# Kernel tuning notes

Measured on AMD Instinct MI355X. Metric: run time of the kernel, lower is better.

## Reference

```python
import jax, jax.numpy as jnp
from jax import lax
import numpy as np

FRAME_LEN = 128
HOP = 64  # frame_len // 2 (default hop)
SAMPLE_LEN = 65536
IR_LEN = 1024

# torch.hann_window(N) is periodic: 0.5*(1 - cos(2*pi*n/N))
WIN = 0.5 * (1.0 - jnp.cos(2.0 * jnp.pi * jnp.arange(FRAME_LEN, dtype=jnp.float32) / FRAME_LEN))


def setup_inputs() -> dict:
    key = jax.random.key(0)
    k1, k2 = jax.random.split(key)
    x = jax.random.normal(k1, (1, SAMPLE_LEN), dtype=jnp.float32)
    IR = jax.random.normal(k2, (1, IR_LEN), dtype=jnp.float32)
    return {"x": x, "IR": IR}


def _scale_ir(ir2d):
    # get_MSG + scale_IR(target_gain = MSG + 2)
    spec = jnp.fft.rfft(ir2d[0])
    mag = jnp.abs(spec)
    phase = jnp.angle(spec)
    power = mag ** 2
    MLG = jnp.mean(power)
    zero_phase = (phase > -0.1) & (phase < 0.1)  # DC bin always qualifies
    peak_gain = jnp.max(jnp.where(zero_phase, power, -jnp.inf))
    MSG = -10.0 * jnp.log10(peak_gain / MLG)
    target_gain = MSG + 2.0
    mean_gain = 10.0 * jnp.log10(MLG)
    factor = jnp.power(jnp.float32(0.5), (target_gain - mean_gain) / 6.0)
    return ir2d / factor


def _howling(x1d, ir1d):
    L = x1d.shape[0]
    conv_len = FRAME_LEN + ir1d.shape[0] - 1
    # number of iterations that perform the feedback update (torch loop breaks
    # when frame_start + conv_len >= sample_len, AFTER adding to howling_out)
    n_fb = max(0, (L - conv_len - 1) // HOP)

    def step(x, i):
        fs = i * HOP
        frame = lax.dynamic_slice(x, (fs,), (FRAME_LEN,))
        w = WIN * frame
        conv = jnp.convolve(w, ir1d)  # mode='full', length conv_len
        fs2 = fs + HOP
        seg = lax.dynamic_slice(x, (fs2,), (conv_len,)) + conv
        x = lax.dynamic_update_slice(x, seg, (fs2,))
        x = jnp.clip(x, -1.0, 1.0)
        return x, w

    x_out, frames = lax.scan(step, x1d, jnp.arange(n_fb))
    # last iteration: windowed frame added to howling_out, then break (no feedback, no clamp)
    fs_last = n_fb * HOP
    last_w = WIN * lax.dynamic_slice(x_out, (fs_last,), (FRAME_LEN,))
    frames = jnp.concatenate([frames, last_w[None, :]], axis=0)  # [T, frame_len]
    T = n_fb + 1
    pos = (jnp.arange(T)[:, None] * HOP + jnp.arange(FRAME_LEN)[None, :]).reshape(-1)
    howl = jnp.zeros((L,), x1d.dtype).at[pos].add(frames.reshape(-1))
    return jnp.clip(howl, -1.0, 1.0)


def reference(x, IR):
    ir = _scale_ir(IR)
    out = _howling(x[0], ir[0])
    return out[None, :]
```

## Files before the change

### kernel.cpp

```cpp
#include <hip/hip_runtime.h>
#include <math.h>

#define FRAME 128
#define HOPW 64
#define SLEN 65536
#define IRLEN 1024
#define NFB 1006
#define RMASK 2047
#define PI_D 3.14159265358979323846

__device__ __forceinline__ float clip1(float v) { return fminf(1.0f, fmaxf(-1.0f, v)); }

__device__ __forceinline__ void loop_barrier() {
    __builtin_amdgcn_sched_barrier(0);
    asm volatile("s_waitcnt lgkmcnt(0)" ::: "memory");
    __builtin_amdgcn_s_barrier();
    __builtin_amdgcn_sched_barrier(0);
}

__global__ __launch_bounds__(768) void howl_fused(const float* __restrict__ x,
                                                  const float* __restrict__ ir,
                                                  float* __restrict__ out) {
    __shared__ float ring[2048];
    __shared__ float part[3][4][1152];
    __shared__ float irl[IRLEN];
    __shared__ float tailb[2][HOPW];
    __shared__ float red1[1024];
    __shared__ float red2[1024];
    __shared__ float invfs;

    const int tid = threadIdx.x;
    const int lane = tid & 63;
    const int wvid = tid >> 6;
    const int kg = tid / 192;
    const int ob = tid % 192;
    const int q = ob * 6;
    const int lo = q - kg * 32 - 31;
    const int s = kg * 32 + (lane & 31);

    for (int idx = tid; idx < IRLEN; idx += 768) irl[idx] = ir[idx];
    for (int idx = tid; idx < 1216; idx += 768) ring[idx] = x[idx];
    if (tid >= 513) { red1[tid] = -INFINITY; red2[tid] = 0.f; }
    if (tid < 256) { red1[768 + tid] = -INFINITY; red2[768 + tid] = 0.f; }
    __syncthreads();

    if (tid < 513) {
        double th = -2.0 * PI_D * (double)tid / 1024.0;
        double c4 = cos(4.0 * th), s4 = sin(4.0 * th);
        double wr0 = 1.0,           wi0 = 0.0;
        double wr1 = cos(th),       wi1 = sin(th);
        double wr2 = cos(2.0 * th), wi2 = sin(2.0 * th);
        double wr3 = cos(3.0 * th), wi3 = sin(3.0 * th);
        double ar0 = 0, ai0 = 0, ar1 = 0, ai1 = 0, ar2 = 0, ai2 = 0, ar3 = 0, ai3 = 0;
        for (int m = 0; m < 256; ++m) {
            double x0 = irl[4 * m], x1 = irl[4 * m + 1], x2 = irl[4 * m + 2], x3 = irl[4 * m + 3];
            ar0 += x0 * wr0; ai0 += x0 * wi0;
            ar1 += x1 * wr1; ai1 += x1 * wi1;
            ar2 += x2 * wr2; ai2 += x2 * wi2;
            ar3 += x3 * wr3; ai3 += x3 * wi3;
            double t;
            t = wr0 * c4 - wi0 * s4; wi0 = wr0 * s4 + wi0 * c4; wr0 = t;
            t = wr1 * c4 - wi1 * s4; wi1 = wr1 * s4 + wi1 * c4; wr1 = t;
            t = wr2 * c4 - wi2 * s4; wi2 = wr2 * s4 + wi2 * c4; wr2 = t;
            t = wr3 * c4 - wi3 * s4; wi3 = wr3 * s4 + wi3 * c4; wr3 = t;
        }
        double re = (ar0 + ar1) + (ar2 + ar3);
        double im = (ai0 + ai1) + (ai2 + ai3);
        float mag = (float)sqrt(re * re + im * im);
        float pw = mag * mag;
        double ph = atan2(im, re);
        int ok = (ph > -0.1 && ph < 0.1) ? 1 : 0;
        red1[tid] = ok ? pw : -INFINITY;
        red2[tid] = pw;
    }
    __syncthreads();
    for (int st = 512; st > 0; st >>= 1) {
        if (tid < st) {
            red1[tid] = fmaxf(red1[tid], red1[tid + st]);
            red2[tid] = red2[tid] + red2[tid + st];
        }
        __syncthreads();
    }
    if (tid == 0) {
        float peak = red1[0];
        float MLG = red2[0] / 513.0f;
        float MSG = -10.0f * log10f(peak / MLG);
        float target_gain = MSG + 2.0f;
        float mean_gain = 10.0f * log10f(MLG);
        invfs = powf(0.5f, (target_gain - mean_gain) / 6.0f);
    }
    __syncthreads();

    const float fbc = invfs;
    float wir[37];
#pragma unroll
    for (int j = 0; j < 37; ++j) {
        int idx = lo + j;
        wir[j] = (idx >= 0 && idx < IRLEN) ? irl[idx] / fbc : 0.f;
    }

    const float hwv = (float)(0.5 * (1.0 - cos(PI_D * (double)s / 64.0)));

    float wreg = hwv * ring[s];
    if ((wvid == 0 || wvid == 3) && lane < 32) out[s] = clip1(wreg);
    if ((wvid == 6 || wvid == 9) && lane < 32) tailb[0][s - 64] = wreg;
    float xv = 0.f;
    if (wvid == 4) xv = x[1216 + lane];
    __syncthreads();

    auto body = [&](int i, float (*cur)[1152], const float (*prev)[1152], int first) {
        const int base = i * HOPW;

        if (wvid == 4) {
            int pos = base + 1216 + lane;
            if (pos < SLEN) ring[pos & RMASK] = clip1(xv);
            int np = pos + HOPW;
            xv = (np < SLEN) ? x[np] : 0.f;
        }

        if (!first && (wvid == 2 || wvid == 5 || wvid == 8 || wvid == 11)) {
            int c = ((wvid - 2) / 3) * 64 + lane;
            int p = 128 + 4 * c;
            float4 g0 = *(const float4*)&prev[0][p];
            float4 g1 = *(const float4*)&prev[1][p];
            float4 g2 = *(const float4*)&prev[2][p];
            float4 g3 = *(const float4*)&prev[3][p];
            int slot = (base + p) & RMASK;
            float4 r = *(float4*)&ring[slot];
            r.x = clip1(r.x + (((g0.x + g1.x) + g2.x) + g3.x));
            r.y = clip1(r.y + (((g0.y + g1.y) + g2.y) + g3.y));
            r.z = clip1(r.z + (((g0.z + g1.z) + g2.z) + g3.z));
            r.w = clip1(r.w + (((g0.w + g1.w) + g2.w) + g3.w));
            *(float4*)&ring[slot] = r;
        }

        float a0 = 0, a1 = 0, a2 = 0, a3 = 0, a4 = 0, a5 = 0;
#pragma unroll
        for (int kk = 0; kk < 32; ++kk) {
            float sc = __int_as_float(__builtin_amdgcn_readlane(__float_as_int(wreg), 31 - kk));
            a0 = fmaf(sc, wir[kk + 0], a0);
            a1 = fmaf(sc, wir[kk + 1], a1);
            a2 = fmaf(sc, wir[kk + 2], a2);
            a3 = fmaf(sc, wir[kk + 3], a3);
            a4 = fmaf(sc, wir[kk + 4], a4);
            a5 = fmaf(sc, wir[kk + 5], a5);
        }
        float* pw = &cur[kg][q];
        *(float2*)(pw + 0) = make_float2(a0, a1);
        *(float2*)(pw + 2) = make_float2(a2, a3);
        *(float2*)(pw + 4) = make_float2(a4, a5);

        loop_barrier();

        float rr = ring[(base + 64 + s) & RMASK];
        float c0 = cur[0][s], c1 = cur[1][s], c2 = cur[2][s], c3 = cur[3][s];
        float sc4 = ((c0 + c1) + c2) + c3;
        if (kg < 2) {
            float v;
            if (first) {
                v = clip1(rr + sc4);
            } else {
                float m0 = prev[0][64 + s], m1 = prev[1][64 + s];
                float m2 = prev[2][64 + s], m3 = prev[3][64 + s];
                float sm = ((m0 + m1) + m2) + m3;
                v = clip1(clip1(rr + sm) + sc4);
            }
            float wn = hwv * v;
            if ((wvid == 0 || wvid == 3) && lane < 32) {
                float told = tailb[i & 1][s];
                out[base + 64 + s] = clip1(wn + told);
            }
            wreg = wn;
        } else {
            float v = clip1(rr + sc4);
            float wn = hwv * v;
            if ((wvid == 6 || wvid == 9) && lane < 32) tailb[(i + 1) & 1][s - 64] = wn;
            wreg = wn;
        }
    };

    float (*P0)[1152] = part[0];
    float (*P1)[1152] = part[1];
    float (*P2)[1152] = part[2];

    body(0, P0, P2, 1);
#pragma unroll 1
    for (int i = 1; i < NFB; i += 3) {
        body(i,     P1, P0, 0);
        body(i + 1, P2, P1, 0);
        body(i + 2, P0, P2, 0);
    }

    if ((wvid == 6 || wvid == 9) && lane < 32) out[64448 + (s - 64)] = clip1(wreg);
    for (int idx = 64512 + tid; idx < SLEN; idx += 768) out[idx] = 0.f;
}

extern "C" void kernel_launch(void* const* d_in, const int* in_sizes, int n_in,
                              void* d_out, int out_size, void* d_ws, size_t ws_size,
                              hipStream_t stream) {
    const float* x = (const float*)d_in[0];
    const float* ir = (const float*)d_in[1];
    float* out = (float*)d_out;
    (void)d_ws; (void)ws_size; (void)in_sizes; (void)n_in; (void)out_size;

    hipLaunchKernelGGL(howl_fused, dim3(1), dim3(768), 0, stream, x, ir, out);
}
```

Before: 1.144 ms.

## Replace triple-buffered single-barrier pipeline with two-barrier loop through LDS

The rotating three-buffer partial-sum scheme, which needed one barrier per step, is replaced by a single partial buffer. Each step now ends with a second barrier, after the ring update and the next windowed frame are written to LDS. The next frame is passed through a shared wlds array instead of staying in registers, the output accumulation moves to wave 0, and waves 0-1 get raised scheduling priority. The code is simpler, but each iteration now has two block-wide barriers on the serial critical path instead of one.

```diff
diff --git a/kernel.cpp b/kernel.cpp
--- a/kernel.cpp
+++ b/kernel.cpp
@@ -21,10 +21,10 @@
 __global__ __launch_bounds__(768) void howl_fused(const float* __restrict__ x,
                                                   const float* __restrict__ ir,
                                                   float* __restrict__ out) {
-    __shared__ float ring[2048];
-    __shared__ float part[3][4][1152];
+    __shared__ __align__(16) float ring[2048];
+    __shared__ __align__(16) float part[4][1152];
     __shared__ float irl[IRLEN];
-    __shared__ float tailb[2][HOPW];
+    __shared__ float wlds[FRAME];
     __shared__ float red1[1024];
     __shared__ float red2[1024];
     __shared__ float invfs;
@@ -36,7 +36,6 @@
     const int ob = tid % 192;
     const int q = ob * 6;
     const int lo = q - kg * 32 - 31;
-    const int s = kg * 32 + (lane & 31);
 
     for (int idx = tid; idx < IRLEN; idx += 768) irl[idx] = ir[idx];
     for (int idx = tid; idx < 1216; idx += 768) ring[idx] = x[idx];
@@ -90,8 +89,8 @@
         invfs = powf(0.5f, (target_gain - mean_gain) / 6.0f);
     }
     __syncthreads();
+    const float fbc = invfs;
 
-    const float fbc = invfs;
     float wir[37];
 #pragma unroll
     for (int j = 0; j < 37; ++j) {
@@ -99,41 +98,31 @@
         wir[j] = (idx >= 0 && idx < IRLEN) ? irl[idx] / fbc : 0.f;
     }
 
-    const float hwv = (float)(0.5 * (1.0 - cos(PI_D * (double)s / 64.0)));
+    const float hvs = (float)(0.5 * (1.0 - cos(PI_D * (double)(tid & 127) / 64.0)));
 
-    float wreg = hwv * ring[s];
-    if ((wvid == 0 || wvid == 3) && lane < 32) out[s] = clip1(wreg);
-    if ((wvid == 6 || wvid == 9) && lane < 32) tailb[0][s - 64] = wreg;
-    float xv = 0.f;
-    if (wvid == 4) xv = x[1216 + lane];
+    float tl = 0.f, xv = 0.f;
+    if (tid < FRAME) wlds[tid] = hvs * ring[tid];
+    if (wvid == 11) xv = x[1216 + lane];
+    if (wvid < 2) __builtin_amdgcn_s_setprio(1);
     __syncthreads();
 
-    auto body = [&](int i, float (*cur)[1152], const float (*prev)[1152], int first) {
+#pragma unroll 1
+    for (int i = 0; i < NFB; ++i) {
         const int base = i * HOPW;
 
-        if (wvid == 4) {
+        if (wvid == 0) {
+            float w0v = wlds[lane];
+            float w1v = wlds[64 + lane];
+            out[base + lane] = clip1(w0v + tl);
+            tl = w1v;
+        } else if (wvid == 11) {
             int pos = base + 1216 + lane;
             if (pos < SLEN) ring[pos & RMASK] = clip1(xv);
             int np = pos + HOPW;
             xv = (np < SLEN) ? x[np] : 0.f;
         }
 
-        if (!first && (wvid == 2 || wvid == 5 || wvid == 8 || wvid == 11)) {
-            int c = ((wvid - 2) / 3) * 64 + lane;
-            int p = 128 + 4 * c;
-            float4 g0 = *(const float4*)&prev[0][p];
-            float4 g1 = *(const float4*)&prev[1][p];
-            float4 g2 = *(const float4*)&prev[2][p];
-            float4 g3 = *(const float4*)&prev[3][p];
-            int slot = (base + p) & RMASK;
-            float4 r = *(float4*)&ring[slot];
-            r.x = clip1(r.x + (((g0.x + g1.x) + g2.x) + g3.x));
-            r.y = clip1(r.y + (((g0.y + g1.y) + g2.y) + g3.y));
-            r.z = clip1(r.z + (((g0.z + g1.z) + g2.z) + g3.z));
-            r.w = clip1(r.w + (((g0.w + g1.w) + g2.w) + g3.w));
-            *(float4*)&ring[slot] = r;
-        }
-
+        float wreg = wlds[kg * 32 + (lane & 31)];
         float a0 = 0, a1 = 0, a2 = 0, a3 = 0, a4 = 0, a5 = 0;
 #pragma unroll
         for (int kk = 0; kk < 32; ++kk) {
@@ -145,53 +134,43 @@
             a4 = fmaf(sc, wir[kk + 4], a4);
             a5 = fmaf(sc, wir[kk + 5], a5);
         }
-        float* pw = &cur[kg][q];
+        float* pw = &part[kg][q];
         *(float2*)(pw + 0) = make_float2(a0, a1);
         *(float2*)(pw + 2) = make_float2(a2, a3);
         *(float2*)(pw + 4) = make_float2(a4, a5);
 
         loop_barrier();
 
-        float rr = ring[(base + 64 + s) & RMASK];
-        float c0 = cur[0][s], c1 = cur[1][s], c2 = cur[2][s], c3 = cur[3][s];
-        float sc4 = ((c0 + c1) + c2) + c3;
-        if (kg < 2) {
-            float v;
-            if (first) {
-                v = clip1(rr + sc4);
-            } else {
-                float m0 = prev[0][64 + s], m1 = prev[1][64 + s];
-                float m2 = prev[2][64 + s], m3 = prev[3][64 + s];
-                float sm = ((m0 + m1) + m2) + m3;
-                v = clip1(clip1(rr + sm) + sc4);
-            }
-            float wn = hwv * v;
-            if ((wvid == 0 || wvid == 3) && lane < 32) {
-                float told = tailb[i & 1][s];
-                out[base + 64 + s] = clip1(wn + told);
-            }
-            wreg = wn;
-        } else {
+        if (tid < 128) {
+            int s = tid;
+            int slot = (base + 64 + s) & RMASK;
+            float rr = ring[slot];
+            float sc4 = ((part[0][s] + part[1][s]) + part[2][s]) + part[3][s];
             float v = clip1(rr + sc4);
-            float wn = hwv * v;
-            if ((wvid == 6 || wvid == 9) && lane < 32) tailb[(i + 1) & 1][s - 64] = wn;
-            wreg = wn;
+            ring[slot] = v;
+            wlds[s] = hvs * v;
+        } else if (tid < 384) {
+            int p = 128 + 4 * (tid - 128);
+            float4 g0 = *(const float4*)&part[0][p];
+            float4 g1 = *(const float4*)&part[1][p];
+            float4 g2 = *(const float4*)&part[2][p];
+            float4 g3 = *(const float4*)&part[3][p];
+            int slot = (base + 64 + p) & RMASK;
+            float4 rv = *(float4*)&ring[slot];
+            rv.x = clip1(rv.x + (((g0.x + g1.x) + g2.x) + g3.x));
+            rv.y = clip1(rv.y + (((g0.y + g1.y) + g2.y) + g3.y));
+            rv.z = clip1(rv.z + (((g0.z + g1.z) + g2.z) + g3.z));
+            rv.w = clip1(rv.w + (((g0.w + g1.w) + g2.w) + g3.w));
+            *(float4*)&ring[slot] = rv;
         }
-    };
 
-    float (*P0)[1152] = part[0];
-    float (*P1)[1152] = part[1];
-    float (*P2)[1152] = part[2];
-
-    body(0, P0, P2, 1);
-#pragma unroll 1
-    for (int i = 1; i < NFB; i += 3) {
-        body(i,     P1, P0, 0);
-        body(i + 1, P2, P1, 0);
-        body(i + 2, P0, P2, 0);
+        loop_barrier();
     }
 
-    if ((wvid == 6 || wvid == 9) && lane < 32) out[64448 + (s - 64)] = clip1(wreg);
+    if (wvid == 0) {
+        out[64384 + lane] = clip1(wlds[lane] + tl);
+        out[64448 + lane] = clip1(wlds[64 + lane]);
+    }
     for (int idx = 64512 + tid; idx < SLEN; idx += 768) out[idx] = 0.f;
 }
 
```

Result: faster. 1.020 ms (-10.9%).
